# Kernel optimization log

Hardware: AMD Instinct MI355X
Metric: run time of the kernel (lower is better)

Reference implementation:

```python
import jax, jax.numpy as jnp
import numpy as np

B, S, H = 8, 2048, 256
MAX_SEQ = 2048


def get_rotary_matrix(context_window, embedding_dim):
    # Faithful to the llama-from-scratch construction (note the (i-1) quirk):
    # theta_i = 10000 ** (-2*(i-1)/d) for i in [0, d/2)
    half = embedding_dim // 2
    i = jnp.arange(half, dtype=jnp.float32)
    theta = jnp.power(10000.0, -2.0 * (i - 1.0) / embedding_dim)  # [half]
    pos = jnp.arange(context_window, dtype=jnp.float32)  # [S]
    ang = pos[:, None] * theta[None, :]  # [S, half]
    c, s = jnp.cos(ang), jnp.sin(ang)
    R = jnp.zeros((context_window, embedding_dim, embedding_dim), dtype=jnp.float32)
    idx = jnp.arange(half)
    R = R.at[:, 2 * idx, 2 * idx].set(c)
    R = R.at[:, 2 * idx, 2 * idx + 1].set(-s)
    R = R.at[:, 2 * idx + 1, 2 * idx].set(s)
    R = R.at[:, 2 * idx + 1, 2 * idx + 1].set(c)
    return R


def setup_inputs() -> dict:
    key = jax.random.key(0)
    kx, kq, kk, kv = jax.random.split(key, 4)
    scale = 1.0 / np.sqrt(H)
    x = jax.random.normal(kx, (B, S, H), dtype=jnp.float32)
    wq = jax.random.uniform(kq, (H, H), dtype=jnp.float32, minval=-scale, maxval=scale)
    wk = jax.random.uniform(kk, (H, H), dtype=jnp.float32, minval=-scale, maxval=scale)
    wv = jax.random.uniform(kv, (H, H), dtype=jnp.float32, minval=-scale, maxval=scale)
    r = get_rotary_matrix(MAX_SEQ, H)
    return {"x": x, "wq": wq, "wk": wk, "wv": wv, "r": r}


def reference(x, wq, wk, wv, r):
    b, s, h = x.shape
    # nn.Linear(bias=False): y = x @ W.T
    q = jnp.einsum("bsh,oh->bso", x, wq)
    k = jnp.einsum("bsh,oh->bso", x, wk)
    v = jnp.einsum("bsh,oh->bso", x, wv)
    # per-position dense rotary rotation: qr[b,s,:] = q[b,s,:] @ r[s]
    rs = r[:s]
    qr = jnp.einsum("bsh,shk->bsk", q, rs)
    kr = jnp.einsum("bsh,shk->bsk", k, rs)
    attn = jnp.einsum("bqh,bkh->bqk", qr, kr) * (h ** -0.5)  # [B,S,S]
    causal = jnp.tril(jnp.ones((s, s), dtype=bool))
    attn = jnp.where(causal[None, :, :], attn, -jnp.inf)
    attn = jax.nn.softmax(attn, axis=-1)
    out = jnp.einsum("bqk,bkh->bqh", attn, v)
    return out
```

## Files before the change

### kernel.cpp

```cpp
#include <hip/hip_runtime.h>


typedef __bf16 bf16x8 __attribute__((ext_vector_type(8)));
typedef float  f32x4  __attribute__((ext_vector_type(4)));
typedef unsigned short u16x4 __attribute__((ext_vector_type(4)));

#define LOG2E 1.44269504088896340736f
#define LOG2_10000 13.287712379549449f

__device__ __forceinline__ unsigned short f2bf(float f) {
    union { __bf16 h; unsigned short u; } cv;
    cv.h = (__bf16)f;
    return cv.u;
}

__device__ __forceinline__ void gl_lds16(const unsigned short* g, unsigned short* lds) {
    __builtin_amdgcn_global_load_lds(
        (const __attribute__((address_space(1))) unsigned int*)g,
        (__attribute__((address_space(3))) unsigned int*)lds, 16, 0, 0);
}

__global__ __launch_bounds__(256) void prep(
    const float* __restrict__ wq, const float* __restrict__ wk,
    const float* __restrict__ wv,
    float2* __restrict__ cs, unsigned short* __restrict__ wb) {
    int bid = blockIdx.x;
    if (bid < 1024) {
        int id = bid * 256 + threadIdx.x;
        int s = id >> 7;
        int i = id & 127;
        float ex = -2.0f * ((float)i - 1.0f) * (1.0f / 256.0f);
        float theta = exp2f(LOG2_10000 * ex);
        float ang = (float)s * theta;
        float sn, c;
        sincosf(ang, &sn, &c);
        cs[id] = make_float2(c, sn);
    } else {
        int id = (bid - 1024) * 256 + threadIdx.x;
        int sel = id >> 14;
        int off = id & 16383;
        const float* src = (sel == 0) ? wq : (sel == 1) ? wk : wv;
        float4 d = ((const float4*)src)[off];
        u16x4 pk = { f2bf(d.x), f2bf(d.y), f2bf(d.z), f2bf(d.w) };
        *(u16x4*)&wb[(size_t)sel * 65536 + (size_t)off * 4] = pk;
    }
}

__global__ __launch_bounds__(256, 2) void qkv_rope(
    const float* __restrict__ x, const unsigned short* __restrict__ wb,
    const float2* __restrict__ cs,
    unsigned short* __restrict__ qr, unsigned short* __restrict__ kr,
    unsigned short* __restrict__ vt) {

    __shared__ unsigned short Ash[32 * 256];
    __shared__ unsigned short Bsh[256 * 64];

    const int mt  = blockIdx.x;
    const int tid = threadIdx.x;
    const int w = tid >> 6, l = tid & 63;
    const int lane_m = l & 15, quad = l >> 4;
    const int wm = w >> 1, wn = w & 1;

#pragma unroll
    for (int p = 0; p < 8; ++p) {
        int id = p * 256 + tid;
        int row = id >> 6, f4 = id & 63;
        float4 d = *(const float4*)(x + (size_t)(mt * 32 + row) * 256 + f4 * 4);
        u16x4 pk = { f2bf(d.x), f2bf(d.y), f2bf(d.z), f2bf(d.w) };
        int k = f4 * 4;
        int idx = row * 256 + ((((k >> 3) ^ row) << 3) | (k & 7));
        *(u16x4*)&Ash[idx] = pk;
    }

    for (int sel = 0; sel < 3; ++sel) {
        f32x4 acc[8];
#pragma unroll
        for (int c = 0; c < 8; ++c) acc[c] = (f32x4){0.f, 0.f, 0.f, 0.f};

        for (int kc = 0; kc < 4; ++kc) {
            __syncthreads();
#pragma unroll
            for (int p = 0; p < 8; ++p) {
                int rb = (p * 4 + w) * 8;
                int rowg = rb + (l >> 3);
                int cg = (l & 7) ^ (rowg & 7);
                gl_lds16(wb + (size_t)sel * 65536 + (size_t)rowg * 256 + kc * 64 + cg * 8,
                         &Bsh[rb * 64]);
            }
            __syncthreads();
#pragma unroll
            for (int ks = 0; ks < 2; ++ks) {
                int ck = kc * 8 + ks * 4 + quad;
                int r0 = wm * 16 + lane_m;
                bf16x8 a0 = *(const bf16x8*)&Ash[r0 * 256 + ((ck ^ r0) << 3)];
#pragma unroll
                for (int ct = 0; ct < 8; ++ct) {
                    int nn = wn * 128 + ct * 16 + lane_m;
                    bf16x8 bb = *(const bf16x8*)&Bsh[nn * 64 + (((ks * 4 + quad) ^ (nn & 7)) << 3)];
                    acc[ct] = __builtin_amdgcn_mfma_f32_16x16x32_bf16(a0, bb, acc[ct], 0, 0, 0);
                }
            }
        }

        int mbase = mt * 32 + wm * 16 + quad * 4;
        if (sel < 2) {
            unsigned short* dst = sel ? kr : qr;
            const float scale = sel ? 1.0f : 0.0625f;
#pragma unroll
            for (int ct = 0; ct < 8; ++ct) {
                int col = wn * 128 + ct * 16 + lane_m;
                int ii = col >> 1;
                float sgn = (col & 1) ? -1.0f : 1.0f;
#pragma unroll
                for (int rr = 0; rr < 4; ++rr) {
                    int m = mbase + rr;
                    int spos = m & 2047;
                    float2 csv = cs[spos * 128 + ii];
                    float v = acc[ct][rr];
                    float pr = __shfl_xor(v, 1);
                    float rot = (csv.x * v + sgn * csv.y * pr) * scale;
                    dst[(size_t)m * 256 + col] = f2bf(rot);
                }
            }
        } else {
#pragma unroll
            for (int ct = 0; ct < 8; ++ct) {
                int col = wn * 128 + ct * 16 + lane_m;
                u16x4 pk = { f2bf(acc[ct][0]), f2bf(acc[ct][1]),
                             f2bf(acc[ct][2]), f2bf(acc[ct][3]) };
                int bb = mbase >> 11;
                int s0 = mbase & 2047;
                *(u16x4*)&vt[((size_t)bb * 256 + col) * 2048 + s0] = pk;
            }
        }
    }
}

__global__ __launch_bounds__(256, 2) void flash_attn(
    const unsigned short* __restrict__ qr, const unsigned short* __restrict__ kr,
    const unsigned short* __restrict__ vt, float* __restrict__ out) {

    __shared__ unsigned short Ksh[64 * 256];
    __shared__ unsigned short Vsh[256 * 64];
    __shared__ unsigned short Psh[32 * 64];

    const int n = blockIdx.x;
    const int b = n & 7;
    const int idx = n >> 3;
    const int j = (idx < 32) ? (63 - idx) : (idx - 32);
    const int q0 = j * 32;

    const int tid = threadIdx.x;
    const int w = tid >> 6, l = tid & 63;
    const int lane_m = l & 15, quad = l >> 4;
    const int qw = w >> 1;
    const int kp = w & 1;

    bf16x8 qf[8];
    {
        const unsigned short* qb =
            qr + ((size_t)(b * 2048 + q0 + qw * 16 + lane_m)) * 256 + quad * 8;
#pragma unroll
        for (int ks = 0; ks < 8; ++ks) qf[ks] = *(const bf16x8*)(qb + ks * 32);
    }

    f32x4 o[16];
#pragma unroll
    for (int t = 0; t < 16; ++t) o[t] = (f32x4){0.f, 0.f, 0.f, 0.f};
    float l_part[4] = {0.f, 0.f, 0.f, 0.f};

    const int nkt = ((q0 + 31) >> 6) + 1;
    const int rmax = q0 + qw * 16 + 15;

    for (int kt = 0; kt < nkt; ++kt) {
        const int kv0 = kt * 64;
        __syncthreads();
#pragma unroll
        for (int p = 0; p < 8; ++p) {
            int rb = (p * 4 + w) * 2;
            int row = rb + (l >> 5);
            int cg = (l & 31) ^ (row & 31);
            gl_lds16(kr + ((size_t)(b * 2048 + kv0 + row)) * 256 + cg * 8, &Ksh[rb * 256]);
        }
#pragma unroll
        for (int p = 0; p < 8; ++p) {
            int hb = (p * 4 + w) * 8;
            int h = hb + (l >> 3);
            int cg = (l & 7) ^ (h & 7);
            gl_lds16(vt + ((size_t)(b * 256 + h)) * 2048 + kv0 + cg * 8, &Vsh[hb * 64]);
        }
        __syncthreads();

        const bool active = (kv0 + 32 * kp) <= rmax;
        if (active) {
            f32x4 sacc[2];
#pragma unroll
            for (int ct = 0; ct < 2; ++ct) sacc[ct] = (f32x4){0.f, 0.f, 0.f, 0.f};
#pragma unroll
            for (int ks = 0; ks < 8; ++ks) {
                bf16x8 a = qf[ks];
#pragma unroll
                for (int ct = 0; ct < 2; ++ct) {
                    int kvr = kp * 32 + ct * 16 + lane_m;
                    bf16x8 bb = *(const bf16x8*)&Ksh[kvr * 256 + (((ks * 4 + quad) ^ (kvr & 31)) << 3)];
                    sacc[ct] = __builtin_amdgcn_mfma_f32_16x16x32_bf16(a, bb, sacc[ct], 0, 0, 0);
                }
            }

            const bool needmask = (kv0 + kp * 32 + 31) > (q0 + qw * 16);
#pragma unroll
            for (int ct = 0; ct < 2; ++ct) {
                int col_l = kp * 32 + ct * 16 + lane_m;
                int col_g = kv0 + col_l;
#pragma unroll
                for (int rr = 0; rr < 4; ++rr) {
                    float e = exp2f(sacc[ct][rr] * LOG2E);
                    if (needmask) {
                        int row_g = q0 + qw * 16 + quad * 4 + rr;
                        if (col_g > row_g) e = 0.0f;
                    }
                    l_part[rr] += e;
                    int row = qw * 16 + quad * 4 + rr;
                    Psh[row * 64 + ((((col_l >> 3) ^ (row & 7)) << 3) | (col_l & 7))] = f2bf(e);
                }
            }

            {
                int prow = qw * 16 + lane_m;
                int pk = kp * 4 + quad;
                bf16x8 a = *(const bf16x8*)&Psh[prow * 64 + ((pk ^ (prow & 7)) << 3)];
#pragma unroll
                for (int ht = 0; ht < 16; ++ht) {
                    int h = ht * 16 + lane_m;
                    bf16x8 bb = *(const bf16x8*)&Vsh[h * 64 + ((pk ^ (h & 7)) << 3)];
                    o[ht] = __builtin_amdgcn_mfma_f32_16x16x32_bf16(a, bb, o[ht], 0, 0, 0);
                }
            }
        }
    }

#pragma unroll
    for (int rr = 0; rr < 4; ++rr) {
        l_part[rr] += __shfl_xor(l_part[rr], 1);
        l_part[rr] += __shfl_xor(l_part[rr], 2);
        l_part[rr] += __shfl_xor(l_part[rr], 4);
        l_part[rr] += __shfl_xor(l_part[rr], 8);
    }

    __syncthreads();
    float* mlbuf = (float*)Vsh;
    float* obuf  = (float*)Ksh;
    if (lane_m == 0) {
#pragma unroll
        for (int rr = 0; rr < 4; ++rr)
            mlbuf[(qw * 2 + kp) * 16 + quad * 4 + rr] = l_part[rr];
    }
    if (kp == 1) {
#pragma unroll
        for (int ht = 0; ht < 16; ++ht)
#pragma unroll
            for (int rr = 0; rr < 4; ++rr)
                obuf[(qw * 16 + quad * 4 + rr) * 256 + ht * 16 + lane_m] = o[ht][rr];
    }
    __syncthreads();
    if (kp == 0) {
        float inv[4];
#pragma unroll
        for (int rr = 0; rr < 4; ++rr)
            inv[rr] = 1.0f / (l_part[rr] + mlbuf[(qw * 2 + 1) * 16 + quad * 4 + rr]);
#pragma unroll
        for (int ht = 0; ht < 16; ++ht) {
#pragma unroll
            for (int rr = 0; rr < 4; ++rr) {
                float val = o[ht][rr] +
                            obuf[(qw * 16 + quad * 4 + rr) * 256 + ht * 16 + lane_m];
                size_t idx2 = ((size_t)(b * 2048 + q0 + qw * 16 + quad * 4 + rr)) * 256
                              + ht * 16 + lane_m;
                out[idx2] = val * inv[rr];
            }
        }
    }
}

extern "C" void kernel_launch(void* const* d_in, const int* in_sizes, int n_in,
                              void* d_out, int out_size, void* d_ws, size_t ws_size,
                              hipStream_t stream) {
    const float* x  = (const float*)d_in[0];
    const float* wq = (const float*)d_in[1];
    const float* wk = (const float*)d_in[2];
    const float* wv = (const float*)d_in[3];
    float* out = (float*)d_out;

    char* ws = (char*)d_ws;
    float2*         cs = (float2*)ws;
    unsigned short* qr = (unsigned short*)(ws + (2u << 20));
    unsigned short* kr = (unsigned short*)(ws + (10u << 20));
    unsigned short* vt = (unsigned short*)(ws + (18u << 20));
    unsigned short* wb = (unsigned short*)(ws + (26u << 20));

    prep<<<dim3(1216), dim3(256), 0, stream>>>(wq, wk, wv, cs, wb);
    qkv_rope<<<dim3(512), dim3(256), 0, stream>>>(x, wb, cs, qr, kr, vt);
    flash_attn<<<dim3(512), dim3(256), 0, stream>>>(qr, kr, vt, out);
}
```

Before: 656.7 us.

## Prefetch next K/V tiles during attention compute and widen weight K-chunks

```diff
diff --git a/kernel.cpp b/kernel.cpp
--- a/kernel.cpp
+++ b/kernel.cpp
@@ -53,7 +53,7 @@
     unsigned short* __restrict__ vt) {
 
     __shared__ unsigned short Ash[32 * 256];
-    __shared__ unsigned short Bsh[256 * 64];
+    __shared__ unsigned short Bsh[256 * 128];
 
     const int mt  = blockIdx.x;
     const int tid = threadIdx.x;
@@ -77,26 +77,27 @@
 #pragma unroll
         for (int c = 0; c < 8; ++c) acc[c] = (f32x4){0.f, 0.f, 0.f, 0.f};
 
-        for (int kc = 0; kc < 4; ++kc) {
+        for (int kc2 = 0; kc2 < 2; ++kc2) {
             __syncthreads();
 #pragma unroll
-            for (int p = 0; p < 8; ++p) {
-                int rb = (p * 4 + w) * 8;
-                int rowg = rb + (l >> 3);
-                int cg = (l & 7) ^ (rowg & 7);
-                gl_lds16(wb + (size_t)sel * 65536 + (size_t)rowg * 256 + kc * 64 + cg * 8,
-                         &Bsh[rb * 64]);
+            for (int p = 0; p < 16; ++p) {
+                int rb = (p * 4 + w) * 4;
+                int rowg = rb + (l >> 4);
+                int cg = (l & 15) ^ (rowg & 15);
+                gl_lds16(wb + (size_t)sel * 65536 + (size_t)rowg * 256 + kc2 * 128 + cg * 8,
+                         &Bsh[rb * 128]);
             }
             __syncthreads();
 #pragma unroll
-            for (int ks = 0; ks < 2; ++ks) {
-                int ck = kc * 8 + ks * 4 + quad;
+            for (int ks = 0; ks < 4; ++ks) {
+                int ck = kc2 * 16 + ks * 4 + quad;
+                int cl = ks * 4 + quad;
                 int r0 = wm * 16 + lane_m;
                 bf16x8 a0 = *(const bf16x8*)&Ash[r0 * 256 + ((ck ^ r0) << 3)];
 #pragma unroll
                 for (int ct = 0; ct < 8; ++ct) {
                     int nn = wn * 128 + ct * 16 + lane_m;
-                    bf16x8 bb = *(const bf16x8*)&Bsh[nn * 64 + (((ks * 4 + quad) ^ (nn & 7)) << 3)];
+                    bf16x8 bb = *(const bf16x8*)&Bsh[nn * 128 + (((cl ^ (nn & 15))) << 3)];
                     acc[ct] = __builtin_amdgcn_mfma_f32_16x16x32_bf16(a0, bb, acc[ct], 0, 0, 0);
                 }
             }
@@ -172,28 +173,30 @@
     const int nkt = ((q0 + 31) >> 6) + 1;
     const int rmax = q0 + qw * 16 + 15;
 
+#pragma unroll
+    for (int p = 0; p < 8; ++p) {
+        int rb = (p * 4 + w) * 2;
+        int row = rb + (l >> 5);
+        int cg = (l & 31) ^ (row & 31);
+        gl_lds16(kr + ((size_t)(b * 2048 + row)) * 256 + cg * 8, &Ksh[rb * 256]);
+    }
+#pragma unroll
+    for (int p = 0; p < 8; ++p) {
+        int hb = (p * 4 + w) * 8;
+        int h = hb + (l >> 3);
+        int cg = (l & 7) ^ (h & 7);
+        gl_lds16(vt + ((size_t)(b * 256 + h)) * 2048 + cg * 8, &Vsh[hb * 64]);
+    }
+
     for (int kt = 0; kt < nkt; ++kt) {
         const int kv0 = kt * 64;
+        const int kv1 = kv0 + 64;
+        const bool more = (kt + 1) < nkt;
         __syncthreads();
-#pragma unroll
-        for (int p = 0; p < 8; ++p) {
-            int rb = (p * 4 + w) * 2;
-            int row = rb + (l >> 5);
-            int cg = (l & 31) ^ (row & 31);
-            gl_lds16(kr + ((size_t)(b * 2048 + kv0 + row)) * 256 + cg * 8, &Ksh[rb * 256]);
-        }
-#pragma unroll
-        for (int p = 0; p < 8; ++p) {
-            int hb = (p * 4 + w) * 8;
-            int h = hb + (l >> 3);
-            int cg = (l & 7) ^ (h & 7);
-            gl_lds16(vt + ((size_t)(b * 256 + h)) * 2048 + kv0 + cg * 8, &Vsh[hb * 64]);
-        }
-        __syncthreads();
 
         const bool active = (kv0 + 32 * kp) <= rmax;
+        f32x4 sacc[2];
         if (active) {
-            f32x4 sacc[2];
 #pragma unroll
             for (int ct = 0; ct < 2; ++ct) sacc[ct] = (f32x4){0.f, 0.f, 0.f, 0.f};
 #pragma unroll
@@ -206,7 +209,20 @@
                     sacc[ct] = __builtin_amdgcn_mfma_f32_16x16x32_bf16(a, bb, sacc[ct], 0, 0, 0);
                 }
             }
-
+        }
+        __syncthreads();
+
+        if (more) {
+#pragma unroll
+            for (int p = 0; p < 8; ++p) {
+                int rb = (p * 4 + w) * 2;
+                int row = rb + (l >> 5);
+                int cg = (l & 31) ^ (row & 31);
+                gl_lds16(kr + ((size_t)(b * 2048 + kv1 + row)) * 256 + cg * 8, &Ksh[rb * 256]);
+            }
+        }
+
+        if (active) {
             const bool needmask = (kv0 + kp * 32 + 31) > (q0 + qw * 16);
 #pragma unroll
             for (int ct = 0; ct < 2; ++ct) {
@@ -224,7 +240,6 @@
                     Psh[row * 64 + ((((col_l >> 3) ^ (row & 7)) << 3) | (col_l & 7))] = f2bf(e);
                 }
             }
-
             {
                 int prow = qw * 16 + lane_m;
                 int pk = kp * 4 + quad;
@@ -235,6 +250,17 @@
                     bf16x8 bb = *(const bf16x8*)&Vsh[h * 64 + ((pk ^ (h & 7)) << 3)];
                     o[ht] = __builtin_amdgcn_mfma_f32_16x16x32_bf16(a, bb, o[ht], 0, 0, 0);
                 }
+            }
+        }
+        __syncthreads();
+
+        if (more) {
+#pragma unroll
+            for (int p = 0; p < 8; ++p) {
+                int hb = (p * 4 + w) * 8;
+                int h = hb + (l >> 3);
+                int cg = (l & 7) ^ (h & 7);
+                gl_lds16(vt + ((size_t)(b * 256 + h)) * 2048 + kv1 + cg * 8, &Vsh[hb * 64]);
             }
         }
     }
```

Measured after the change: 649.4 us. About the same (-1.1%).
